# Kernel tuning notes

Measured on AMD Instinct MI355X. Metric: run time of the kernel, lower is better.

Reference implementation:

```python
import jax, jax.numpy as jnp
import numpy as np

A = 1.0          # jacobi a
B = 1.0          # jacobi b
BASE_ALPHA = 2.0
K = 10           # polynomial order
N = 16384        # nodes
C = 32           # channels


def setup_inputs() -> dict:
    key = jax.random.key(0)
    k1, k2 = jax.random.split(key, 2)
    x = jax.random.normal(k1, (N, C), dtype=jnp.float32)
    # dense graph operator (stand-in for a normalized laplacian); scaled so spectrum is O(1)
    L = jax.random.normal(k2, (N, N), dtype=jnp.float32) / np.float32(np.sqrt(N))
    conv_params = jnp.full((K + 1,), min(1.0 / BASE_ALPHA, 1.0), dtype=jnp.float32)
    comb_params = jnp.ones((K + 1, C), dtype=jnp.float32)
    return {"x": x, "L": L, "conv_params": conv_params, "comb_params": comb_params}


def reference(x, L, conv_params, comb_params):
    a, b = A, B
    alpha = BASE_ALPHA * jnp.tanh(conv_params)  # [K+1] learned step sizes
    polys = [x]  # P_0 = x
    if K >= 1:
        # with l=-1, r=1: (r+l)/(r-l)=0, 1/(r-l)=0.5
        c1 = alpha[0] * (a - b) / 2.0
        c2 = alpha[0] * (a + b + 2.0) / 2.0
        polys.append(c1 * x + c2 * (L @ x))
    for i in range(2, K + 1):
        div = 2.0 * i * (i + a + b) * (2.0 * i + a + b - 2.0)
        r1 = (2.0 * i + a + b) * (2.0 * i + a + b - 1.0) * (2.0 * i + a + b - 2.0) / div
        r2 = (2.0 * i + a + b - 1.0) * (a * a - b * b) / div
        r3 = 2.0 * (i + a - 1.0) * (i + b - 1.0) * (2.0 * i + a + b) / div
        c1 = alpha[i - 1] * r1                      # multiplies L @ P_{i-1} (coef1, since 2/(r-l)=1)
        c2 = alpha[i - 1] * r2                      # coef2 (the (r+l)/(r-l) term vanishes)
        c3 = alpha[i - 1] * alpha[i - 2] * r3       # coef_3
        polys.append(c1 * (L @ polys[-1]) + c2 * polys[-1] - c3 * polys[-2])
    # y = sum_k comb[k] (broadcast over nodes) * P_k  -- avoids materializing the stacked [K+1,N,C]
    y = polys[0] * comb_params[0][None, :]
    for k in range(1, K + 1):
        y = y + comb_params[k][None, :] * polys[k]
    return y
```

## Files before the change

kernel.cpp:

```cpp
#include <hip/hip_runtime.h>
#include <math.h>


#define NN 16384
#define CC 32
#define KPOLY 10
#define NSPLIT 16
#define KSEG (NN / NSPLIT)
#define STEPS (KSEG / 32)
#define NTK (NN / 32)

typedef _Float16 half8 __attribute__((ext_vector_type(8)));
typedef float f32x4 __attribute__((ext_vector_type(4)));
typedef unsigned int u32x4 __attribute__((ext_vector_type(4)));
typedef unsigned int u32x2 __attribute__((ext_vector_type(2)));

union U16 {
  u32x4 u;
  half8 h;
};
union H4 {
  _Float16 h[4];
  u32x2 u;
};

__global__ __launch_bounds__(256) void conv_L_pack(const float* __restrict__ L,
                                                   _Float16* __restrict__ Lf) {
  __shared__ _Float16 lds[16 * 1024];
  const int tid = threadIdx.x;
  const int tr = blockIdx.x >> 4;
  const int sc = blockIdx.x & 15;
  const float* src = L + (size_t)tr * 16 * NN + (size_t)sc * 1024;

#pragma unroll
  for (int j = 0; j < 16; ++j) {
    const int flat = j * 256 + tid;
    const int r = flat >> 8;
    const int cu = flat & 255;
    f32x4 v = __builtin_nontemporal_load(
        reinterpret_cast<const f32x4*>(src + (size_t)r * NN) + cu);
    H4 o;
    o.h[0] = (_Float16)v.x;
    o.h[1] = (_Float16)v.y;
    o.h[2] = (_Float16)v.z;
    o.h[3] = (_Float16)v.w;
    const int u = (cu >> 1) ^ (r & 7);
    *reinterpret_cast<u32x2*>(&lds[r * 1024 + u * 8 + (cu & 1) * 4]) = o.u;
  }
  __syncthreads();

  const int lane = tid & 63;
  const int wave = tid >> 6;
  const int r = lane & 15;
  const int lg = lane >> 4;
#pragma unroll
  for (int i = 0; i < 8; ++i) {
    const int tkl = wave * 8 + i;
    const int u = (tkl * 4 + lg) ^ (r & 7);
    u32x4 val = *reinterpret_cast<const u32x4*>(&lds[r * 1024 + u * 8]);
    const size_t tk = (size_t)sc * 32 + tkl;
    __builtin_nontemporal_store(
        val, reinterpret_cast<u32x4*>(Lf + ((size_t)tr * NTK + tk) * 512) + lane);
  }
}

__global__ __launch_bounds__(256, 4) void gemm_f16(const _Float16* __restrict__ Lf,
                                                   const _Float16* __restrict__ Ph,
                                                   float* __restrict__ part) {
  const int tid = threadIdx.x;
  const int lane = tid & 63;
  const int wave = tid >> 6;
  const int rg = blockIdx.x & 63;
  const int split = blockIdx.x >> 6;
  const int rb = rg * 256 + wave * 64;
  const int k0 = split * KSEG;
  const int tk0 = k0 >> 5;
  const int l15 = lane & 15;
  const int lg = lane >> 4;

  const u32x4* Ap[4];
#pragma unroll
  for (int rt = 0; rt < 4; ++rt)
    Ap[rt] = reinterpret_cast<const u32x4*>(
                 Lf + ((size_t)((rb >> 4) + rt) * NTK + tk0) * 512) +
             lane;
  const u32x4* Bp[2];
#pragma unroll
  for (int ct = 0; ct < 2; ++ct)
    Bp[ct] = reinterpret_cast<const u32x4*>(Ph + (size_t)(k0 / 8 + lg) * 256 +
                                            (size_t)(ct * 16 + l15) * 8);

  f32x4 acc[4][2];
#pragma unroll
  for (int rt = 0; rt < 4; ++rt)
#pragma unroll
    for (int ct = 0; ct < 2; ++ct) acc[rt][ct] = (f32x4){0.f, 0.f, 0.f, 0.f};

  U16 A[2][4], B[2][2];
#pragma unroll
  for (int rt = 0; rt < 4; ++rt) A[0][rt].u = __builtin_nontemporal_load(Ap[rt]);
#pragma unroll
  for (int ct = 0; ct < 2; ++ct) B[0][ct].u = *Bp[ct];

#pragma unroll
  for (int kk = 0; kk < STEPS; ++kk) {
    const int cur = kk & 1;
    const int nxt = cur ^ 1;
    if (kk < STEPS - 1) {
#pragma unroll
      for (int rt = 0; rt < 4; ++rt)
        A[nxt][rt].u = __builtin_nontemporal_load(Ap[rt] + (kk + 1) * 64);
#pragma unroll
      for (int ct = 0; ct < 2; ++ct)
        B[nxt][ct].u = *reinterpret_cast<const u32x4*>(
            reinterpret_cast<const _Float16*>(Bp[ct]) + 1024 * (kk + 1));
    }
#pragma unroll
    for (int rt = 0; rt < 4; ++rt)
#pragma unroll
      for (int ct = 0; ct < 2; ++ct)
        acc[rt][ct] = __builtin_amdgcn_mfma_f32_16x16x32_f16(A[cur][rt].h, B[cur][ct].h,
                                                             acc[rt][ct], 0, 0, 0);
  }

  float* pb = part + (size_t)split * NN * CC;
#pragma unroll
  for (int rt = 0; rt < 4; ++rt)
#pragma unroll
    for (int ct = 0; ct < 2; ++ct)
#pragma unroll
      for (int j = 0; j < 4; ++j)
        pb[(size_t)(rb + rt * 16 + lg * 4 + j) * CC + ct * 16 + l15] = acc[rt][ct][j];
}

__global__ __launch_bounds__(256) void init_kernel(const float* __restrict__ x,
                                                   const float* __restrict__ comb,
                                                   float* __restrict__ y,
                                                   _Float16* __restrict__ Ph) {
  int idx = blockIdx.x * blockDim.x + threadIdx.x;
  float4 xv = reinterpret_cast<const float4*>(x)[idx];
  int c4 = (idx & 7) << 2;
  int n = idx >> 3;
  float4 cb = *reinterpret_cast<const float4*>(comb + c4);
  reinterpret_cast<float4*>(y)[idx] =
      make_float4(xv.x * cb.x, xv.y * cb.y, xv.z * cb.z, xv.w * cb.w);
  size_t pb = (size_t)(n >> 3) * 256 + (size_t)c4 * 8 + (n & 7);
  Ph[pb] = (_Float16)xv.x;
  Ph[pb + 8] = (_Float16)xv.y;
  Ph[pb + 16] = (_Float16)xv.z;
  Ph[pb + 24] = (_Float16)xv.w;
}

__global__ __launch_bounds__(256) void poly_update(
    const float* __restrict__ part, float* __restrict__ Pnew,
    const float* __restrict__ Pprev, const float* __restrict__ Pprev2,
    float* __restrict__ y, _Float16* __restrict__ Ph, const float* __restrict__ conv,
    const float* __restrict__ comb_row, float r1, float r2, float r3, int ia, int ib,
    int has2) {
  int idx = blockIdx.x * blockDim.x + threadIdx.x;
  float a1 = 2.f * tanhf(conv[ia]);
  float cL = a1 * r1;
  float cP = a1 * r2;

  float4 t = make_float4(0.f, 0.f, 0.f, 0.f);
#pragma unroll
  for (int s = 0; s < NSPLIT; ++s) {
    float4 p = reinterpret_cast<const float4*>(part)[(size_t)s * (NN * CC / 4) + idx];
    t.x += p.x;
    t.y += p.y;
    t.z += p.z;
    t.w += p.w;
  }

  float4 pp = reinterpret_cast<const float4*>(Pprev)[idx];
  float4 pn;
  pn.x = cL * t.x + cP * pp.x;
  pn.y = cL * t.y + cP * pp.y;
  pn.z = cL * t.z + cP * pp.z;
  pn.w = cL * t.w + cP * pp.w;
  if (has2) {
    float a2 = 2.f * tanhf(conv[ib]);
    float cPP = a1 * a2 * r3;
    float4 p2 = reinterpret_cast<const float4*>(Pprev2)[idx];
    pn.x -= cPP * p2.x;
    pn.y -= cPP * p2.y;
    pn.z -= cPP * p2.z;
    pn.w -= cPP * p2.w;
  }
  reinterpret_cast<float4*>(Pnew)[idx] = pn;

  int c4 = (idx & 7) << 2;
  int n = idx >> 3;
  size_t pb = (size_t)(n >> 3) * 256 + (size_t)c4 * 8 + (n & 7);
  Ph[pb] = (_Float16)pn.x;
  Ph[pb + 8] = (_Float16)pn.y;
  Ph[pb + 16] = (_Float16)pn.z;
  Ph[pb + 24] = (_Float16)pn.w;

  float4 cb = *reinterpret_cast<const float4*>(comb_row + c4);
  float4 yv = reinterpret_cast<float4*>(y)[idx];
  yv.x = fmaf(cb.x, pn.x, yv.x);
  yv.y = fmaf(cb.y, pn.y, yv.y);
  yv.z = fmaf(cb.z, pn.z, yv.z);
  yv.w = fmaf(cb.w, pn.w, yv.w);
  reinterpret_cast<float4*>(y)[idx] = yv;
}

static void jacobi_r(int i, double a, double b, float& r1, float& r2, float& r3) {
  double div = 2.0 * i * (i + a + b) * (2.0 * i + a + b - 2.0);
  r1 = (float)((2.0 * i + a + b) * (2.0 * i + a + b - 1.0) * (2.0 * i + a + b - 2.0) / div);
  r2 = (float)((2.0 * i + a + b - 1.0) * (a * a - b * b) / div);
  r3 = (float)(2.0 * (i + a - 1.0) * (i + b - 1.0) * (2.0 * i + a + b) / div);
}

extern "C" void kernel_launch(void* const* d_in, const int* in_sizes, int n_in,
                              void* d_out, int out_size, void* d_ws, size_t ws_size,
                              hipStream_t stream) {
  const float* x = (const float*)d_in[0];
  const float* Lm = (const float*)d_in[1];
  const float* conv = (const float*)d_in[2];
  const float* comb = (const float*)d_in[3];
  float* y = (float*)d_out;
  char* ws = (char*)d_ws;

  _Float16* Lf = (_Float16*)ws;
  float* part = (float*)(ws + 536870912ull);
  _Float16* Ph = (_Float16*)(ws + 536870912ull + 33554432ull);
  float* Pb0 = (float*)(ws + 536870912ull + 33554432ull + 2097152ull);
  float* Pb1 = Pb0 + (size_t)NN * CC;
  float* Pb2 = Pb1 + (size_t)NN * CC;
  float* bufs[3] = {Pb0, Pb1, Pb2};

  const double Aj = 1.0, Bj = 1.0;
  const int ew_blocks = NN * CC / 4 / 256;

  conv_L_pack<<<16384, 256, 0, stream>>>(Lm, Lf);
  init_kernel<<<ew_blocks, 256, 0, stream>>>(x, comb, y, Ph);

  const float* Pprev = x;
  const float* Pprev2 = x;
  for (int i = 1; i <= KPOLY; ++i) {
    gemm_f16<<<64 * NSPLIT, 256, 0, stream>>>(Lf, Ph, part);

    float r1, r2, r3;
    if (i == 1) {
      r1 = (float)((Aj + Bj + 2.0) / 2.0);
      r2 = (float)((Aj - Bj) / 2.0);
      r3 = 0.f;
    } else {
      jacobi_r(i, Aj, Bj, r1, r2, r3);
    }
    float* Pn = bufs[(i - 1) % 3];
    poly_update<<<ew_blocks, 256, 0, stream>>>(part, Pn, Pprev, Pprev2, y, Ph, conv,
                                               comb + (size_t)i * CC, r1, r2, r3, i - 1,
                                               (i >= 2) ? i - 2 : 0, (i >= 2) ? 1 : 0);
    Pprev2 = Pprev;
    Pprev = Pn;
  }
}
```

Measured before the change: 1.380 ms.

## Fuse first L@x product into the fp32-to-fp16 L packing kernel

The conversion kernel now also multiplies each freshly packed 16x1024 tile of L by the fp16 x slice with MFMA, reduces the four waves' partials in shared memory, and writes the split-K partial sums directly. The separate first GEMM launch is dropped, so L is not re-read from memory for the first polynomial. In exchange, init must run before the pack kernel, and the pack kernel does extra Ph loads and an LDS reduction with additional barriers.

Result: faster. 1.276 ms (-7.5%).

```diff
diff --git a/kernel.cpp b/kernel.cpp
--- a/kernel.cpp
+++ b/kernel.cpp
@@ -24,9 +24,11 @@
   u32x2 u;
 };
 
-__global__ __launch_bounds__(256) void conv_L_pack(const float* __restrict__ L,
-                                                   _Float16* __restrict__ Lf) {
-  __shared__ _Float16 lds[16 * 1024];
+__global__ __launch_bounds__(256) void conv_pack_gemm1(const float* __restrict__ L,
+                                                       _Float16* __restrict__ Lf,
+                                                       const _Float16* __restrict__ Ph,
+                                                       float* __restrict__ part) {
+  __shared__ __align__(16) _Float16 lds[16 * 1024];
   const int tid = threadIdx.x;
   const int tr = blockIdx.x >> 4;
   const int sc = blockIdx.x & 15;
@@ -53,15 +55,42 @@
   const int wave = tid >> 6;
   const int r = lane & 15;
   const int lg = lane >> 4;
+
+  f32x4 acc0 = (f32x4){0.f, 0.f, 0.f, 0.f};
+  f32x4 acc1 = (f32x4){0.f, 0.f, 0.f, 0.f};
 #pragma unroll
   for (int i = 0; i < 8; ++i) {
     const int tkl = wave * 8 + i;
     const int u = (tkl * 4 + lg) ^ (r & 7);
-    u32x4 val = *reinterpret_cast<const u32x4*>(&lds[r * 1024 + u * 8]);
+    U16 aval;
+    aval.u = *reinterpret_cast<const u32x4*>(&lds[r * 1024 + u * 8]);
     const size_t tk = (size_t)sc * 32 + tkl;
     __builtin_nontemporal_store(
-        val, reinterpret_cast<u32x4*>(Lf + ((size_t)tr * NTK + tk) * 512) + lane);
-  }
+        aval.u, reinterpret_cast<u32x4*>(Lf + ((size_t)tr * NTK + tk) * 512) + lane);
+    const int kb = sc * 128 + tkl * 4 + lg;
+    U16 b0, b1;
+    b0.u = *reinterpret_cast<const u32x4*>(Ph + (size_t)kb * 256 + (size_t)r * 8);
+    b1.u = *reinterpret_cast<const u32x4*>(Ph + (size_t)kb * 256 + (size_t)(16 + r) * 8);
+    acc0 = __builtin_amdgcn_mfma_f32_16x16x32_f16(aval.h, b0.h, acc0, 0, 0, 0);
+    acc1 = __builtin_amdgcn_mfma_f32_16x16x32_f16(aval.h, b1.h, acc1, 0, 0, 0);
+  }
+  __syncthreads();
+
+  float* red = reinterpret_cast<float*>(lds);
+#pragma unroll
+  for (int j = 0; j < 4; ++j) {
+    red[wave * 512 + (lg * 4 + j) * 32 + r] = acc0[j];
+    red[wave * 512 + (lg * 4 + j) * 32 + 16 + r] = acc1[j];
+  }
+  __syncthreads();
+
+  const int e = tid * 2;
+  float2 s0 = *reinterpret_cast<const float2*>(&red[e]);
+  float2 s1 = *reinterpret_cast<const float2*>(&red[512 + e]);
+  float2 s2 = *reinterpret_cast<const float2*>(&red[1024 + e]);
+  float2 s3 = *reinterpret_cast<const float2*>(&red[1536 + e]);
+  float2 s = make_float2(s0.x + s1.x + s2.x + s3.x, s0.y + s1.y + s2.y + s3.y);
+  *reinterpret_cast<float2*>(part + (size_t)sc * NN * CC + (size_t)tr * 16 * CC + e) = s;
 }
 
 __global__ __launch_bounds__(256, 4) void gemm_f16(const _Float16* __restrict__ Lf,
@@ -234,13 +263,13 @@
   const double Aj = 1.0, Bj = 1.0;
   const int ew_blocks = NN * CC / 4 / 256;
 
-  conv_L_pack<<<16384, 256, 0, stream>>>(Lm, Lf);
   init_kernel<<<ew_blocks, 256, 0, stream>>>(x, comb, y, Ph);
+  conv_pack_gemm1<<<16384, 256, 0, stream>>>(Lm, Lf, Ph, part);
 
   const float* Pprev = x;
   const float* Pprev2 = x;
   for (int i = 1; i <= KPOLY; ++i) {
-    gemm_f16<<<64 * NSPLIT, 256, 0, stream>>>(Lf, Ph, part);
+    if (i > 1) gemm_f16<<<64 * NSPLIT, 256, 0, stream>>>(Lf, Ph, part);
 
     float r1, r2, r3;
     if (i == 1) {
```
